# Optimization experiments

Measured on AMD Instinct MI355X. Metric: run time of the kernel, lower is better.

The kernel has to match this reference:

```python
import jax, jax.numpy as jnp
import numpy as np

N_TASK = 50000
N_PROC = 256
N_EDGES = 800000
EMB = 64
HEADS = 4
NLAYERS = 3
EDIM = 8
TDIM = 16
PDIM = 8
NGRAPHS = 8


def setup_inputs():
    key = jax.random.key(0)
    ks = jax.random.split(key, 30)

    def nrm(k, shape, fan_in):
        return jax.random.normal(k, shape, jnp.float32) / np.float32(np.sqrt(fan_in))

    inp = {}
    inp["x_task"] = jax.random.normal(ks[0], (N_TASK, TDIM), jnp.float32)
    inp["x_proc"] = jax.random.normal(ks[1], (N_PROC, PDIM), jnp.float32)
    inp["edge_index"] = jax.random.randint(ks[2], (2, N_EDGES), 0, N_TASK, dtype=jnp.int32)
    inp["edge_attr"] = jax.random.uniform(ks[3], (N_EDGES, EDIM), jnp.float32)
    inp["task_batch"] = jnp.sort(jax.random.randint(ks[4], (N_TASK,), 0, NGRAPHS, dtype=jnp.int32))
    inp["proc_batch"] = jnp.sort(jax.random.randint(ks[5], (N_PROC,), 0, NGRAPHS, dtype=jnp.int32))
    # input embeds
    inp["W_task"] = nrm(ks[6], (TDIM, EMB), TDIM)
    inp["b_task"] = jnp.zeros((EMB,), jnp.float32)
    inp["W_proc"] = nrm(ks[7], (PDIM, EMB), PDIM)
    inp["b_proc"] = jnp.zeros((EMB,), jnp.float32)
    # per-layer GAT params (stacked over layers)
    inp["gat_W"] = nrm(ks[8], (NLAYERS, EMB, HEADS * EMB), EMB)
    inp["gat_We"] = nrm(ks[9], (NLAYERS, EDIM, HEADS * EMB), EDIM)
    inp["att_src"] = nrm(ks[10], (NLAYERS, HEADS, EMB), EMB)
    inp["att_dst"] = nrm(ks[11], (NLAYERS, HEADS, EMB), EMB)
    inp["att_edge"] = nrm(ks[12], (NLAYERS, HEADS, EMB), EMB)
    inp["gat_b"] = jnp.zeros((NLAYERS, HEADS * EMB), jnp.float32)
    inp["proj_W"] = nrm(ks[13], (NLAYERS, HEADS * EMB, EMB), HEADS * EMB)
    inp["proj_b"] = jnp.zeros((NLAYERS, EMB), jnp.float32)
    inp["ln_g"] = jnp.ones((NLAYERS, EMB), jnp.float32)
    inp["ln_b"] = jnp.zeros((NLAYERS, EMB), jnp.float32)
    # heads
    inp["pt_W1"] = nrm(ks[14], (EMB, EMB // 2), EMB)
    inp["pt_b1"] = jnp.zeros((EMB // 2,), jnp.float32)
    inp["pt_W2"] = nrm(ks[15], (EMB // 2, 1), EMB // 2)
    inp["pt_b2"] = jnp.zeros((1,), jnp.float32)
    inp["v_W1"] = nrm(ks[16], (2 * EMB, EMB), 2 * EMB)
    inp["v_b1"] = jnp.zeros((EMB,), jnp.float32)
    inp["v_W2"] = nrm(ks[17], (EMB, 1), EMB)
    inp["v_b2"] = jnp.zeros((1,), jnp.float32)
    return inp


def _gat_layer(x, src, dst, eattr, W, We, a_s, a_d, a_e, bias):
    # PyG GATConv(in=-1 shared lin, heads=H, concat=True, edge_dim) with self loops already appended
    n = x.shape[0]
    xl = (x @ W).reshape(n, HEADS, EMB)            # [N,H,D]
    el = (eattr @ We).reshape(-1, HEADS, EMB)      # [E,H,D]
    a_src = jnp.einsum("nhd,hd->nh", xl, a_s)
    a_dst = jnp.einsum("nhd,hd->nh", xl, a_d)
    a_edg = jnp.einsum("ehd,hd->eh", el, a_e)
    alpha = jax.nn.leaky_relu(a_src[src] + a_dst[dst] + a_edg, 0.2)  # [E,H]
    m = jax.ops.segment_max(alpha, dst, num_segments=n)
    ex = jnp.exp(alpha - m[dst])
    denom = jax.ops.segment_sum(ex, dst, num_segments=n)
    coeff = ex / (denom[dst] + 1e-16)
    out = jax.ops.segment_sum(coeff[:, :, None] * xl[src], dst, num_segments=n)
    return out.reshape(n, HEADS * EMB) + bias


def _mean_pool(x, batch, g):
    s = jax.ops.segment_sum(x, batch, num_segments=g)
    cnt = jax.ops.segment_sum(jnp.ones((x.shape[0], 1), x.dtype), batch, num_segments=g)
    return s / jnp.maximum(cnt, 1.0)


def reference(x_task, x_proc, edge_attr, W_task, b_task, W_proc, b_proc, gat_W, gat_We,
              att_src, att_dst, att_edge, gat_b, proj_W, proj_b, ln_g, ln_b,
              pt_W1, pt_b1, pt_W2, pt_b2, v_W1, v_b1, v_W2, v_b2,
              edge_index, task_batch, proc_batch):
    h_t = x_task @ W_task + b_task
    h_p = x_proc @ W_proc + b_proc
    # add self loops; self-loop edge_attr = mean of edge_attr (PyG fill_value='mean')
    loop = jnp.arange(N_TASK, dtype=edge_index.dtype)
    src = jnp.concatenate([edge_index[0], loop])
    dst = jnp.concatenate([edge_index[1], loop])
    ea = jnp.concatenate([edge_attr, jnp.broadcast_to(edge_attr.mean(0), (N_TASK, EDIM))], axis=0)
    for l in range(NLAYERS):
        upd = _gat_layer(h_t, src, dst, ea, gat_W[l], gat_We[l], att_src[l], att_dst[l], att_edge[l], gat_b[l])
        upd = jax.nn.elu(upd @ proj_W[l] + proj_b[l])
        h = h_t + upd
        mu = h.mean(-1, keepdims=True)
        var = ((h - mu) ** 2).mean(-1, keepdims=True)
        h_t = (h - mu) / jnp.sqrt(var + 1e-5) * ln_g[l] + ln_b[l]
    task_logits = (jax.nn.relu(h_t @ pt_W1 + pt_b1) @ pt_W2 + pt_b2)[:, 0]
    tp = _mean_pool(h_t, task_batch, NGRAPHS)
    pp = _mean_pool(h_p, proc_batch, NGRAPHS)
    ge = jnp.concatenate([tp, pp], axis=1)
    value = jax.nn.relu(ge @ v_W1 + v_b1) @ v_W2 + v_b2
    return task_logits, value, h_t, h_p
```

## Files before the change

kernel.cpp:

```cpp
#include <hip/hip_runtime.h>
#include <hip/hip_bf16.h>
#include <math.h>

#define NT 50000
#define NP 256
#define NE 800000
#define ET 850000
#define EMBD 64
#define NHEADS 4
#define HE 256
#define NG 8
#define NBLK 49

typedef __attribute__((ext_vector_type(8))) short bf16x8;
typedef __attribute__((ext_vector_type(4))) float f32x4;

#define OFF_DEG    0u
#define OFF_INDPTR 200192u
#define OFF_CURSOR 400384u
#define OFF_BLKSUM 600576u
#define OFF_MG     600832u
#define OFF_MH     601216u
#define OFF_MEAN   601280u
#define OFF_TPSUM  601344u
#define OFF_TPCNT  603392u
#define OFF_SRCS   603648u
#define OFF_AE0    4003648u
#define OFF_AE1    17603648u
#define OFF_AE2    31203648u
#define OFF_ASRC   44803648u
#define OFF_ADST   45604416u
#define OFF_HT     46405184u
#define OFF_HTB    59217472u
#define OFF_XL     65623616u
#define OFF_AGG    91223616u
#define OFF_WXF    116848192u
#define OFF_WPF    116946496u

__device__ __forceinline__ float bf_lo(unsigned int u) {
  union { unsigned int i; float f; } v; v.i = u << 16; return v.f;
}
__device__ __forceinline__ float bf_hi(unsigned int u) {
  union { unsigned int i; float f; } v; v.i = u & 0xffff0000u; return v.f;
}

__global__ __launch_bounds__(256) void k_embed_task(const float* __restrict__ x,
    const float* __restrict__ W, const float* __restrict__ b,
    float* __restrict__ ht, __hip_bfloat16* __restrict__ htb) {
  int lane = threadIdx.x & 63, wid = threadIdx.x >> 6;
  float breg[16];
  #pragma unroll
  for (int k = 0; k < 16; k++) breg[k] = W[k * 64 + lane];
  float bias = b[lane];
  int row0 = blockIdx.x * 64 + wid * 16;
  #pragma unroll 1
  for (int r = 0; r < 16; r++) {
    int row = row0 + r;
    if (row >= NT) return;
    const float4* xr = (const float4*)(x + (size_t)row * 16);
    float acc = bias;
    #pragma unroll
    for (int q = 0; q < 4; q++) {
      float4 v = xr[q];
      acc += v.x * breg[q*4+0] + v.y * breg[q*4+1] + v.z * breg[q*4+2] + v.w * breg[q*4+3];
    }
    ht[(size_t)row * 64 + lane] = acc;
    htb[(size_t)row * 64 + lane] = __float2bfloat16(acc);
  }
}

__global__ __launch_bounds__(256) void k_degree_mean(const int* __restrict__ ei1,
    const float* __restrict__ ea, int* __restrict__ deg, float* __restrict__ sums) {
  __shared__ float lds[256];
  int tid = threadIdx.x;
  int e = blockIdx.x * 256 + tid;
  if (e < ET) {
    int d = (e < NE) ? ei1[e] : (e - NE);
    atomicAdd(&deg[d], 1);
  }
  int k = tid & 7, rl = tid >> 3;
  float s = 0.f;
  for (int row = blockIdx.x * 32 + rl; row < NE; row += gridDim.x * 32)
    s += ea[(size_t)row * 8 + k];
  lds[tid] = s;
  __syncthreads();
  for (int off = 128; off >= 8; off >>= 1) {
    if (tid < off) lds[tid] += lds[tid + off];
    __syncthreads();
  }
  if (tid < 8) atomicAdd(&sums[tid], lds[tid]);
}

__global__ __launch_bounds__(1024) void k_scanA(const int* __restrict__ deg,
    int* __restrict__ indptr, int* __restrict__ blksum) {
  __shared__ int wsum[16];
  int tid = threadIdx.x, lane = tid & 63, wid = tid >> 6;
  int i = blockIdx.x * 1024 + tid;
  int v = (i < NT) ? deg[i] : 0;
  int x = v;
  #pragma unroll
  for (int off = 1; off < 64; off <<= 1) {
    int t = __shfl_up(x, off, 64);
    if (lane >= off) x += t;
  }
  if (lane == 63) wsum[wid] = x;
  __syncthreads();
  if (wid == 0 && lane < 16) {
    int w = wsum[lane];
    #pragma unroll
    for (int off = 1; off < 16; off <<= 1) {
      int t = __shfl_up(w, off, 64);
      if (lane >= off) w += t;
    }
    wsum[lane] = w;
  }
  __syncthreads();
  int woff = (wid == 0) ? 0 : wsum[wid - 1];
  if (i < NT) indptr[i] = x + woff - v;
  if (tid == 1023) blksum[blockIdx.x] = wsum[15];
}

__global__ __launch_bounds__(1024) void k_scanB(const int* __restrict__ blksum,
    int* __restrict__ indptr, int* __restrict__ cursor) {
  __shared__ int bs[NBLK];
  int tid = threadIdx.x;
  if (tid < NBLK) bs[tid] = blksum[tid];
  __syncthreads();
  int off = 0;
  for (int j = 0; j < (int)blockIdx.x; j++) off += bs[j];
  int i = blockIdx.x * 1024 + tid;
  if (i < NT) {
    int e = indptr[i] + off;
    indptr[i] = e;
    cursor[i] = e;
  }
  if (blockIdx.x == 0 && tid == 0) {
    int tot = 0;
    for (int j = 0; j < NBLK; j++) tot += bs[j];
    indptr[NT] = tot;
  }
}

__global__ __launch_bounds__(128) void k_mprep(const float* __restrict__ We,
    const float* __restrict__ ae, const float* __restrict__ msum,
    float* __restrict__ Mg, float* __restrict__ Mh) {
  int t = threadIdx.x;
  if (t < 96) {
    int l = t >> 5, idx = t & 31, k = idx >> 2, h = idx & 3;
    const float* Wl = We + (size_t)l * 8 * HE;
    const float* al = ae + (size_t)l * NHEADS * EMBD;
    float s = 0.f;
    #pragma unroll
    for (int d = 0; d < 64; d++) s += Wl[k * HE + h * 64 + d] * al[h * 64 + d];
    Mg[t] = s;
  }
  __syncthreads();
  if (t < 12) {
    int l = t >> 2, h = t & 3;
    float m = 0.f;
    #pragma unroll
    for (int k = 0; k < 8; k++) m += msum[k] * (1.f / NE) * Mg[l * 32 + k * 4 + h];
    Mh[t] = m;
  }
}

__global__ __launch_bounds__(256) void k_fill(const int* __restrict__ ei0,
    const int* __restrict__ ei1, const float* __restrict__ ea,
    const float* __restrict__ Mg, const float* __restrict__ Mh,
    int* __restrict__ cursor, int* __restrict__ srcs,
    float4* __restrict__ ae0, float4* __restrict__ ae1, float4* __restrict__ ae2) {
  __shared__ float MgS[96];
  __shared__ float MhS[12];
  int t = threadIdx.x;
  if (t < 96) MgS[t] = Mg[t];
  if (t < 12) MhS[t] = Mh[t];
  __syncthreads();
  int e = blockIdx.x * 256 + t;
  if (e >= ET) return;
  int d, s;
  float4 r[3];
  if (e < NE) {
    d = ei1[e]; s = ei0[e];
    const float4* pp = (const float4*)(ea + (size_t)e * 8);
    float4 v0 = pp[0], v1 = pp[1];
    float v[8] = {v0.x, v0.y, v0.z, v0.w, v1.x, v1.y, v1.z, v1.w};
    #pragma unroll
    for (int l = 0; l < 3; l++) {
      float rr[4];
      #pragma unroll
      for (int h = 0; h < 4; h++) {
        float acc = 0.f;
        #pragma unroll
        for (int k = 0; k < 8; k++) acc += v[k] * MgS[l * 32 + k * 4 + h];
        rr[h] = acc;
      }
      r[l].x = rr[0]; r[l].y = rr[1]; r[l].z = rr[2]; r[l].w = rr[3];
    }
  } else {
    d = e - NE; s = d;
    #pragma unroll
    for (int l = 0; l < 3; l++) {
      r[l].x = MhS[l * 4 + 0]; r[l].y = MhS[l * 4 + 1];
      r[l].z = MhS[l * 4 + 2]; r[l].w = MhS[l * 4 + 3];
    }
  }
  int p = atomicAdd(&cursor[d], 1);
  srcs[p] = s;
  ae0[p] = r[0];
  ae1[p] = r[1];
  ae2[p] = r[2];
}

__global__ void k_prep_w(const float* __restrict__ Wx, const float* __restrict__ Wp,
                         __hip_bfloat16* __restrict__ Wxf, __hip_bfloat16* __restrict__ Wpf) {
  int lane = threadIdx.x;
  int bid = blockIdx.x;
  int quad = lane >> 4, l15 = lane & 15;
  if (bid < 96) {
    int l = bid >> 5, rem = bid & 31, t = rem >> 1, kb = rem & 1;
    const float* Wl = Wx + (size_t)l * 64 * 256;
    __hip_bfloat16* out = Wxf + (size_t)l * 16384 + (size_t)((t * 2 + kb) * 64 + lane) * 8;
    #pragma unroll
    for (int j = 0; j < 8; j++)
      out[j] = __float2bfloat16(Wl[(kb * 32 + quad * 8 + j) * 256 + t * 16 + l15]);
  } else {
    bid -= 96;
    int l = bid >> 5, rem = bid & 31, t = rem >> 3, kb = rem & 7;
    const float* Wl = Wp + (size_t)l * 256 * 64;
    __hip_bfloat16* out = Wpf + (size_t)l * 16384 + (size_t)((t * 8 + kb) * 64 + lane) * 8;
    #pragma unroll
    for (int j = 0; j < 8; j++)
      out[j] = __float2bfloat16(Wl[(kb * 32 + quad * 8 + j) * 64 + t * 16 + l15]);
  }
}

__global__ __launch_bounds__(256) void k_xl_mfma(
    const __hip_bfloat16* __restrict__ htb, const __hip_bfloat16* __restrict__ Wf,
    const float* __restrict__ as, const float* __restrict__ ad,
    __hip_bfloat16* __restrict__ xl, float* __restrict__ a_src, float* __restrict__ a_dst) {
  int lane = threadIdx.x & 63, wave = threadIdx.x >> 6;
  int quad = lane >> 4, l15 = lane & 15;
  int r0 = blockIdx.x * 64 + wave * 16;
  f32x4 acc[16];
  #pragma unroll
  for (int t = 0; t < 16; t++) acc[t] = (f32x4){0.f, 0.f, 0.f, 0.f};
  #pragma unroll
  for (int kb = 0; kb < 2; kb++) {
    bf16x8 a = *(const bf16x8*)(htb + (size_t)(r0 + l15) * 64 + kb * 32 + quad * 8);
    #pragma unroll
    for (int t = 0; t < 16; t++) {
      bf16x8 bfr = *(const bf16x8*)(Wf + (size_t)((t * 2 + kb) * 64 + lane) * 8);
      acc[t] = __builtin_amdgcn_mfma_f32_16x16x32_bf16(a, bfr, acc[t], 0, 0, 0);
    }
  }
  float asv[16], adv[16];
  #pragma unroll
  for (int t = 0; t < 16; t++) { asv[t] = as[t * 16 + l15]; adv[t] = ad[t * 16 + l15]; }
  #pragma unroll
  for (int reg = 0; reg < 4; reg++) {
    int row = r0 + quad * 4 + reg;
    bool ok = row < NT;
    float vs[4] = {0.f, 0.f, 0.f, 0.f}, vd[4] = {0.f, 0.f, 0.f, 0.f};
    #pragma unroll
    for (int t = 0; t < 16; t++) {
      float v = acc[t][reg];
      if (ok) xl[(size_t)row * HE + t * 16 + l15] = __float2bfloat16(v);
      vs[t >> 2] += v * asv[t];
      vd[t >> 2] += v * adv[t];
    }
    #pragma unroll
    for (int off = 8; off; off >>= 1) {
      #pragma unroll
      for (int h = 0; h < 4; h++) {
        vs[h] += __shfl_xor(vs[h], off, 64);
        vd[h] += __shfl_xor(vd[h], off, 64);
      }
    }
    if (ok && l15 == 0) {
      float4 s4; s4.x = vs[0]; s4.y = vs[1]; s4.z = vs[2]; s4.w = vs[3];
      float4 d4; d4.x = vd[0]; d4.y = vd[1]; d4.z = vd[2]; d4.w = vd[3];
      *(float4*)(a_src + (size_t)row * 4) = s4;
      *(float4*)(a_dst + (size_t)row * 4) = d4;
    }
  }
}

__global__ __launch_bounds__(256) void k_attn(
    const __hip_bfloat16* __restrict__ xl, const float* __restrict__ a_src,
    const float* __restrict__ a_dst, const float* __restrict__ aedg,
    const int* __restrict__ indptr, const int* __restrict__ srcs,
    const float* __restrict__ gb, __hip_bfloat16* __restrict__ agg) {
  int node = blockIdx.x * 4 + (threadIdx.x >> 6);
  int lane = threadIdx.x & 63;
  int h = lane >> 4;
  int hbase = lane & 48;
  int e15 = lane & 15;
  int beg = indptr[node], end = indptr[node + 1];
  float adh = a_dst[node * 4 + h];
  float M = -1e30f, S = 0.f;
  float acc0 = 0.f, acc1 = 0.f, acc2 = 0.f, acc3 = 0.f;
  for (int base = beg; base < end; base += 16) {
    int cnt = min(16, end - base);
    int el = base + e15;
    bool ok = e15 < cnt;
    int my_src = ok ? srcs[el] : 0;
    float aeh = ok ? aedg[(size_t)el * 4 + h] : 0.f;
    float asr = ok ? a_src[(size_t)my_src * 4 + h] : 0.f;
    float al = asr + adh + aeh;
    al = (al > 0.f) ? al : 0.2f * al;
    if (!ok) al = -1e30f;
    float cm = al;
    #pragma unroll
    for (int off = 1; off < 16; off <<= 1) cm = fmaxf(cm, __shfl_xor(cm, off, 64));
    float newM = fmaxf(M, cm);
    float corr = __expf(M - newM);
    float ex = __expf(al - newM);
    float cs = ex;
    #pragma unroll
    for (int off = 1; off < 16; off <<= 1) cs += __shfl_xor(cs, off, 64);
    S = S * corr + cs;
    M = newM;
    acc0 *= corr; acc1 *= corr; acc2 *= corr; acc3 *= corr;
    if (cnt == 16) {
      #pragma unroll 4
      for (int j = 0; j < 16; j++) {
        int src = __shfl(my_src, j, 64);
        float cf = __shfl(ex, hbase | j, 64);
        uint2 u = *(const uint2*)(xl + (size_t)src * HE + lane * 4);
        acc0 += cf * bf_lo(u.x);
        acc1 += cf * bf_hi(u.x);
        acc2 += cf * bf_lo(u.y);
        acc3 += cf * bf_hi(u.y);
      }
    } else {
      for (int j = 0; j < cnt; j++) {
        int src = __shfl(my_src, j, 64);
        float cf = __shfl(ex, hbase | j, 64);
        uint2 u = *(const uint2*)(xl + (size_t)src * HE + lane * 4);
        acc0 += cf * bf_lo(u.x);
        acc1 += cf * bf_hi(u.x);
        acc2 += cf * bf_lo(u.y);
        acc3 += cf * bf_hi(u.y);
      }
    }
  }
  float inv = 1.f / (S + 1e-16f);
  float4 g4 = *(const float4*)(gb + lane * 4);
  unsigned int o0 = __bfloat16_as_ushort(__float2bfloat16(acc0 * inv + g4.x));
  unsigned int o1 = __bfloat16_as_ushort(__float2bfloat16(acc1 * inv + g4.y));
  unsigned int o2 = __bfloat16_as_ushort(__float2bfloat16(acc2 * inv + g4.z));
  unsigned int o3 = __bfloat16_as_ushort(__float2bfloat16(acc3 * inv + g4.w));
  uint2 out; out.x = o0 | (o1 << 16); out.y = o2 | (o3 << 16);
  *(uint2*)(agg + (size_t)node * HE + lane * 4) = out;
}

__global__ __launch_bounds__(256) void k_proj_mfma(
    const __hip_bfloat16* __restrict__ agg, const __hip_bfloat16* __restrict__ Wf,
    const float* __restrict__ pb, const float* __restrict__ g, const float* __restrict__ b,
    const float* __restrict__ ht_in, float* __restrict__ ht_out,
    __hip_bfloat16* __restrict__ htb_out, int writebf) {
  int lane = threadIdx.x & 63, wave = threadIdx.x >> 6;
  int quad = lane >> 4, l15 = lane & 15;
  int r0 = blockIdx.x * 64 + wave * 16;
  f32x4 acc[4];
  #pragma unroll
  for (int t = 0; t < 4; t++) acc[t] = (f32x4){0.f, 0.f, 0.f, 0.f};
  #pragma unroll
  for (int kb = 0; kb < 8; kb++) {
    bf16x8 a = *(const bf16x8*)(agg + (size_t)(r0 + l15) * HE + kb * 32 + quad * 8);
    #pragma unroll
    for (int t = 0; t < 4; t++) {
      bf16x8 bfr = *(const bf16x8*)(Wf + (size_t)((t * 8 + kb) * 64 + lane) * 8);
      acc[t] = __builtin_amdgcn_mfma_f32_16x16x32_bf16(a, bfr, acc[t], 0, 0, 0);
    }
  }
  float pbv[4], gv[4], bv[4];
  #pragma unroll
  for (int t = 0; t < 4; t++) {
    pbv[t] = pb[t * 16 + l15];
    gv[t] = g[t * 16 + l15];
    bv[t] = b[t * 16 + l15];
  }
  #pragma unroll
  for (int reg = 0; reg < 4; reg++) {
    int row = r0 + quad * 4 + reg;
    bool ok = row < NT;
    float h[4], rs = 0.f;
    #pragma unroll
    for (int t = 0; t < 4; t++) {
      float u = acc[t][reg] + pbv[t];
      u = (u > 0.f) ? u : (__expf(u) - 1.f);
      h[t] = ht_in[(size_t)row * 64 + t * 16 + l15] + u;
      rs += h[t];
    }
    #pragma unroll
    for (int off = 8; off; off >>= 1) rs += __shfl_xor(rs, off, 64);
    float mu = rs * 0.015625f;
    float vv = 0.f;
    #pragma unroll
    for (int t = 0; t < 4; t++) { float d = h[t] - mu; vv += d * d; }
    #pragma unroll
    for (int off = 8; off; off >>= 1) vv += __shfl_xor(vv, off, 64);
    float rstd = rsqrtf(vv * 0.015625f + 1e-5f);
    #pragma unroll
    for (int t = 0; t < 4; t++) {
      float o = (h[t] - mu) * rstd * gv[t] + bv[t];
      if (ok) {
        ht_out[(size_t)row * 64 + t * 16 + l15] = o;
        if (writebf) htb_out[(size_t)row * 64 + t * 16 + l15] = __float2bfloat16(o);
      }
    }
  }
}

__global__ __launch_bounds__(256) void k_task_head(const float* __restrict__ ht,
    const float* __restrict__ W1, const float* __restrict__ b1,
    const float* __restrict__ W2, const float* __restrict__ b2, float* __restrict__ logits) {
  __shared__ float lh[8 * 64];
  int t = threadIdx.x;
  size_t base = (size_t)blockIdx.x * 8 * 64;
  lh[t] = ht[base + t];
  lh[t + 256] = ht[base + t + 256];
  __syncthreads();
  int i = t >> 5, j = t & 31;
  float s = b1[j];
  #pragma unroll 8
  for (int d = 0; d < 64; d++) s += lh[i * 64 + d] * W1[d * 32 + j];
  s = fmaxf(s, 0.f);
  float p = s * W2[j];
  #pragma unroll
  for (int off = 16; off; off >>= 1) p += __shfl_xor(p, off, 64);
  if (j == 0) logits[blockIdx.x * 8 + i] = p + b2[0];
}

__global__ __launch_bounds__(256) void k_pool_task(const float* __restrict__ ht,
    const int* __restrict__ tb, float* __restrict__ sums, float* __restrict__ cnt) {
  int lane = threadIdx.x & 63, sub = threadIdx.x >> 6;
  float acc[8], c[8];
  #pragma unroll
  for (int g = 0; g < 8; g++) { acc[g] = 0.f; c[g] = 0.f; }
  int lim = min(NT, (int)((blockIdx.x + 1) * 512));
  for (int n = blockIdx.x * 512 + sub; n < lim; n += 4) {
    int g = tb[n];
    float v = ht[(size_t)n * 64 + lane];
    #pragma unroll
    for (int gg = 0; gg < 8; gg++) {
      if (g == gg) { acc[gg] += v; c[gg] += 1.f; }
    }
  }
  #pragma unroll
  for (int g = 0; g < 8; g++) {
    if (__any(acc[g] != 0.f || c[g] != 0.f)) {
      atomicAdd(&sums[g * 64 + lane], acc[g]);
      if (lane == 0) atomicAdd(&cnt[g], c[g]);
    }
  }
}

__global__ __launch_bounds__(512) void k_value(const float* __restrict__ tpsum,
    const float* __restrict__ tpcnt, const float* __restrict__ x_proc,
    const float* __restrict__ W_proc, const float* __restrict__ b_proc,
    float* __restrict__ hp_out, const int* __restrict__ pbatch,
    const float* __restrict__ vW1, const float* __restrict__ vb1,
    const float* __restrict__ vW2, const float* __restrict__ vb2,
    float* __restrict__ val_out) {
  __shared__ float ge[8 * 128];
  int t = threadIdx.x;
  int g = t >> 6, d = t & 63;
  float wreg[8];
  #pragma unroll
  for (int k = 0; k < 8; k++) wreg[k] = W_proc[k * 64 + d];
  float bd = b_proc[d];
  for (int p = g; p < 256; p += 8) {
    const float* xr = x_proc + (size_t)p * 8;
    float a = bd;
    #pragma unroll
    for (int k = 0; k < 8; k++) a += xr[k] * wreg[k];
    hp_out[(size_t)p * 64 + d] = a;
  }
  __syncthreads();
  float c = fmaxf(tpcnt[g], 1.f);
  ge[g * 128 + d] = tpsum[g * 64 + d] / c;
  float s = 0.f, cc = 0.f;
  for (int p = 0; p < 256; p++) {
    int bg = pbatch[p];
    if (bg == g) { s += hp_out[(size_t)p * 64 + d]; cc += 1.f; }
  }
  ge[g * 128 + 64 + d] = s / fmaxf(cc, 1.f);
  __syncthreads();
  float acc = vb1[d];
  #pragma unroll 8
  for (int k = 0; k < 128; k++) acc += ge[g * 128 + k] * vW1[k * 64 + d];
  acc = fmaxf(acc, 0.f);
  float p = acc * vW2[d];
  #pragma unroll
  for (int off = 32; off; off >>= 1) p += __shfl_xor(p, off, 64);
  if (d == 0) val_out[g] = p + vb2[0];
}

extern "C" void kernel_launch(void* const* d_in, const int* in_sizes, int n_in,
                              void* d_out, int out_size, void* d_ws, size_t ws_size,
                              hipStream_t stream) {
  (void)in_sizes; (void)n_in; (void)out_size; (void)ws_size;
  const float* x_task  = (const float*)d_in[0];
  const float* x_proc  = (const float*)d_in[1];
  const int*   eidx    = (const int*)d_in[2];
  const float* eattr   = (const float*)d_in[3];
  const int*   tbatch  = (const int*)d_in[4];
  const int*   pbatch  = (const int*)d_in[5];
  const float* W_task  = (const float*)d_in[6];
  const float* b_task  = (const float*)d_in[7];
  const float* W_proc  = (const float*)d_in[8];
  const float* b_proc  = (const float*)d_in[9];
  const float* gat_W   = (const float*)d_in[10];
  const float* gat_We  = (const float*)d_in[11];
  const float* att_src = (const float*)d_in[12];
  const float* att_dst = (const float*)d_in[13];
  const float* att_edge= (const float*)d_in[14];
  const float* gat_b   = (const float*)d_in[15];
  const float* proj_W  = (const float*)d_in[16];
  const float* proj_b  = (const float*)d_in[17];
  const float* ln_g    = (const float*)d_in[18];
  const float* ln_b    = (const float*)d_in[19];
  const float* pt_W1   = (const float*)d_in[20];
  const float* pt_b1   = (const float*)d_in[21];
  const float* pt_W2   = (const float*)d_in[22];
  const float* pt_b2   = (const float*)d_in[23];
  const float* v_W1    = (const float*)d_in[24];
  const float* v_b1    = (const float*)d_in[25];
  const float* v_W2    = (const float*)d_in[26];
  const float* v_b2    = (const float*)d_in[27];

  char* ws = (char*)d_ws;
  int*   deg    = (int*)(ws + OFF_DEG);
  int*   indptr = (int*)(ws + OFF_INDPTR);
  int*   cursor = (int*)(ws + OFF_CURSOR);
  int*   blksum = (int*)(ws + OFF_BLKSUM);
  float* Mg     = (float*)(ws + OFF_MG);
  float* Mh     = (float*)(ws + OFF_MH);
  float* msum   = (float*)(ws + OFF_MEAN);
  float* tpsum  = (float*)(ws + OFF_TPSUM);
  float* tpcnt  = (float*)(ws + OFF_TPCNT);
  int*   srcs   = (int*)(ws + OFF_SRCS);
  float4* ae0   = (float4*)(ws + OFF_AE0);
  float4* ae1   = (float4*)(ws + OFF_AE1);
  float4* ae2   = (float4*)(ws + OFF_AE2);
  float* a_src  = (float*)(ws + OFF_ASRC);
  float* a_dst  = (float*)(ws + OFF_ADST);
  float* ht     = (float*)(ws + OFF_HT);
  __hip_bfloat16* htb = (__hip_bfloat16*)(ws + OFF_HTB);
  __hip_bfloat16* xl  = (__hip_bfloat16*)(ws + OFF_XL);
  __hip_bfloat16* agg = (__hip_bfloat16*)(ws + OFF_AGG);
  __hip_bfloat16* wxf = (__hip_bfloat16*)(ws + OFF_WXF);
  __hip_bfloat16* wpf = (__hip_bfloat16*)(ws + OFF_WPF);
  float* aedg[3] = {(float*)ae0, (float*)ae1, (float*)ae2};

  float* out_logits = (float*)d_out;
  float* out_value  = (float*)d_out + NT;
  float* out_ht     = (float*)d_out + NT + NG;
  float* out_hp     = (float*)d_out + NT + NG + (size_t)NT * EMBD;

  hipMemsetAsync(ws + OFF_DEG, 0, NT * 4, stream);
  hipMemsetAsync(ws + OFF_MEAN, 0, 2144, stream);

  k_embed_task<<<782, 256, 0, stream>>>(x_task, W_task, b_task, ht, htb);
  k_degree_mean<<<(ET + 255) / 256, 256, 0, stream>>>(eidx + NE, eattr, deg, msum);
  k_scanA<<<NBLK, 1024, 0, stream>>>(deg, indptr, blksum);
  k_scanB<<<NBLK, 1024, 0, stream>>>(blksum, indptr, cursor);
  k_mprep<<<1, 128, 0, stream>>>(gat_We, att_edge, msum, Mg, Mh);
  k_fill<<<(ET + 255) / 256, 256, 0, stream>>>(eidx, eidx + NE, eattr, Mg, Mh,
                                               cursor, srcs, ae0, ae1, ae2);
  k_prep_w<<<192, 64, 0, stream>>>(gat_W, proj_W, wxf, wpf);

  for (int l = 0; l < 3; l++) {
    k_xl_mfma<<<782, 256, 0, stream>>>(htb, wxf + (size_t)l * 16384,
                                       att_src + l * NHEADS * EMBD,
                                       att_dst + l * NHEADS * EMBD,
                                       xl, a_src, a_dst);
    k_attn<<<NT / 4, 256, 0, stream>>>(xl, a_src, a_dst, aedg[l], indptr, srcs,
                                       gat_b + l * HE, agg);
    float* htout = (l == 2) ? out_ht : ht;
    k_proj_mfma<<<782, 256, 0, stream>>>(agg, wpf + (size_t)l * 16384,
                                         proj_b + l * EMBD, ln_g + l * EMBD,
                                         ln_b + l * EMBD, ht, htout, htb,
                                         (l == 2) ? 0 : 1);
  }

  k_task_head<<<NT / 8, 256, 0, stream>>>(out_ht, pt_W1, pt_b1, pt_W2, pt_b2, out_logits);
  k_pool_task<<<(NT + 511) / 512, 256, 0, stream>>>(out_ht, tbatch, tpsum, tpcnt);
  k_value<<<1, 512, 0, stream>>>(tpsum, tpcnt, x_proc, W_proc, b_proc, out_hp,
                                 pbatch, v_W1, v_b1, v_W2, v_b2, out_value);
}
```

Baseline: 719.8 us.

## Pack edge src and bf16 logits into one record; stage MFMA outputs through LDS

```diff
diff --git a/kernel.cpp b/kernel.cpp
--- a/kernel.cpp
+++ b/kernel.cpp
@@ -24,24 +24,28 @@
 #define OFF_MEAN   601280u
 #define OFF_TPSUM  601344u
 #define OFF_TPCNT  603392u
-#define OFF_SRCS   603648u
-#define OFF_AE0    4003648u
-#define OFF_AE1    17603648u
-#define OFF_AE2    31203648u
-#define OFF_ASRC   44803648u
-#define OFF_ADST   45604416u
-#define OFF_HT     46405184u
-#define OFF_HTB    59217472u
-#define OFF_XL     65623616u
-#define OFF_AGG    91223616u
-#define OFF_WXF    116848192u
-#define OFF_WPF    116946496u
+#define OFF_ER0    603648u
+#define OFF_ER1    14203648u
+#define OFF_ER2    27803648u
+#define OFF_ASRC   41403648u
+#define OFF_ADST   42204416u
+#define OFF_HT     43005184u
+#define OFF_HTB    55817472u
+#define OFF_XL     62223616u
+#define OFF_AGG    87823616u
+#define OFF_WXF    113448192u
+#define OFF_WPF    113546496u
 
 __device__ __forceinline__ float bf_lo(unsigned int u) {
   union { unsigned int i; float f; } v; v.i = u << 16; return v.f;
 }
 __device__ __forceinline__ float bf_hi(unsigned int u) {
   union { unsigned int i; float f; } v; v.i = u & 0xffff0000u; return v.f;
+}
+__device__ __forceinline__ unsigned pk2(float a, float b) {
+  unsigned ua = __bfloat16_as_ushort(__float2bfloat16(a));
+  unsigned ub = __bfloat16_as_ushort(__float2bfloat16(b));
+  return ua | (ub << 16);
 }
 
 __global__ __launch_bounds__(256) void k_embed_task(const float* __restrict__ x,
@@ -167,8 +171,8 @@
 __global__ __launch_bounds__(256) void k_fill(const int* __restrict__ ei0,
     const int* __restrict__ ei1, const float* __restrict__ ea,
     const float* __restrict__ Mg, const float* __restrict__ Mh,
-    int* __restrict__ cursor, int* __restrict__ srcs,
-    float4* __restrict__ ae0, float4* __restrict__ ae1, float4* __restrict__ ae2) {
+    int* __restrict__ cursor,
+    uint4* __restrict__ er0, uint4* __restrict__ er1, uint4* __restrict__ er2) {
   __shared__ float MgS[96];
   __shared__ float MhS[12];
   int t = threadIdx.x;
@@ -178,7 +182,7 @@
   int e = blockIdx.x * 256 + t;
   if (e >= ET) return;
   int d, s;
-  float4 r[3];
+  float r[3][4];
   if (e < NE) {
     d = ei1[e]; s = ei0[e];
     const float4* pp = (const float4*)(ea + (size_t)e * 8);
@@ -186,29 +190,27 @@
     float v[8] = {v0.x, v0.y, v0.z, v0.w, v1.x, v1.y, v1.z, v1.w};
     #pragma unroll
     for (int l = 0; l < 3; l++) {
-      float rr[4];
       #pragma unroll
       for (int h = 0; h < 4; h++) {
         float acc = 0.f;
         #pragma unroll
         for (int k = 0; k < 8; k++) acc += v[k] * MgS[l * 32 + k * 4 + h];
-        rr[h] = acc;
+        r[l][h] = acc;
       }
-      r[l].x = rr[0]; r[l].y = rr[1]; r[l].z = rr[2]; r[l].w = rr[3];
     }
   } else {
     d = e - NE; s = d;
     #pragma unroll
-    for (int l = 0; l < 3; l++) {
-      r[l].x = MhS[l * 4 + 0]; r[l].y = MhS[l * 4 + 1];
-      r[l].z = MhS[l * 4 + 2]; r[l].w = MhS[l * 4 + 3];
-    }
+    for (int l = 0; l < 3; l++)
+      #pragma unroll
+      for (int h = 0; h < 4; h++) r[l][h] = MhS[l * 4 + h];
   }
   int p = atomicAdd(&cursor[d], 1);
-  srcs[p] = s;
-  ae0[p] = r[0];
-  ae1[p] = r[1];
-  ae2[p] = r[2];
+  uint4 rc;
+  rc.x = (unsigned)s; rc.w = 0u;
+  rc.y = pk2(r[0][0], r[0][1]); rc.z = pk2(r[0][2], r[0][3]); er0[p] = rc;
+  rc.y = pk2(r[1][0], r[1][1]); rc.z = pk2(r[1][2], r[1][3]); er1[p] = rc;
+  rc.y = pk2(r[2][0], r[2][1]); rc.z = pk2(r[2][2], r[2][3]); er2[p] = rc;
 }
 
 __global__ void k_prep_w(const float* __restrict__ Wx, const float* __restrict__ Wp,
@@ -238,58 +240,71 @@
     const __hip_bfloat16* __restrict__ htb, const __hip_bfloat16* __restrict__ Wf,
     const float* __restrict__ as, const float* __restrict__ ad,
     __hip_bfloat16* __restrict__ xl, float* __restrict__ a_src, float* __restrict__ a_dst) {
-  int lane = threadIdx.x & 63, wave = threadIdx.x >> 6;
+  __shared__ __hip_bfloat16 cbuf[64 * 264];
+  __shared__ float asL[256], adL[256];
+  int tid = threadIdx.x;
+  int lane = tid & 63, wave = tid >> 6;
   int quad = lane >> 4, l15 = lane & 15;
-  int r0 = blockIdx.x * 64 + wave * 16;
+  asL[tid] = as[tid];
+  adL[tid] = ad[tid];
+  int r0 = blockIdx.x * 64;
+  int arow = r0 + wave * 16 + l15;
   f32x4 acc[16];
   #pragma unroll
   for (int t = 0; t < 16; t++) acc[t] = (f32x4){0.f, 0.f, 0.f, 0.f};
   #pragma unroll
   for (int kb = 0; kb < 2; kb++) {
-    bf16x8 a = *(const bf16x8*)(htb + (size_t)(r0 + l15) * 64 + kb * 32 + quad * 8);
+    bf16x8 a = *(const bf16x8*)(htb + (size_t)arow * 64 + kb * 32 + quad * 8);
     #pragma unroll
     for (int t = 0; t < 16; t++) {
       bf16x8 bfr = *(const bf16x8*)(Wf + (size_t)((t * 2 + kb) * 64 + lane) * 8);
       acc[t] = __builtin_amdgcn_mfma_f32_16x16x32_bf16(a, bfr, acc[t], 0, 0, 0);
     }
   }
-  float asv[16], adv[16];
-  #pragma unroll
-  for (int t = 0; t < 16; t++) { asv[t] = as[t * 16 + l15]; adv[t] = ad[t * 16 + l15]; }
-  #pragma unroll
-  for (int reg = 0; reg < 4; reg++) {
-    int row = r0 + quad * 4 + reg;
-    bool ok = row < NT;
-    float vs[4] = {0.f, 0.f, 0.f, 0.f}, vd[4] = {0.f, 0.f, 0.f, 0.f};
-    #pragma unroll
-    for (int t = 0; t < 16; t++) {
-      float v = acc[t][reg];
-      if (ok) xl[(size_t)row * HE + t * 16 + l15] = __float2bfloat16(v);
-      vs[t >> 2] += v * asv[t];
-      vd[t >> 2] += v * adv[t];
-    }
-    #pragma unroll
-    for (int off = 8; off; off >>= 1) {
-      #pragma unroll
-      for (int h = 0; h < 4; h++) {
-        vs[h] += __shfl_xor(vs[h], off, 64);
-        vd[h] += __shfl_xor(vd[h], off, 64);
-      }
-    }
-    if (ok && l15 == 0) {
-      float4 s4; s4.x = vs[0]; s4.y = vs[1]; s4.z = vs[2]; s4.w = vs[3];
-      float4 d4; d4.x = vd[0]; d4.y = vd[1]; d4.z = vd[2]; d4.w = vd[3];
-      *(float4*)(a_src + (size_t)row * 4) = s4;
-      *(float4*)(a_dst + (size_t)row * 4) = d4;
+  int rloc = wave * 16 + quad * 4;
+  #pragma unroll
+  for (int t = 0; t < 16; t++) {
+    #pragma unroll
+    for (int reg = 0; reg < 4; reg++)
+      cbuf[(rloc + reg) * 264 + t * 16 + l15] = __float2bfloat16(acc[t][reg]);
+  }
+  __syncthreads();
+  {
+    int r = tid & 63, q = tid >> 6;
+    const __hip_bfloat16* rowp = &cbuf[r * 264 + q * 64];
+    float vs = 0.f, vd = 0.f;
+    #pragma unroll
+    for (int d8 = 0; d8 < 8; d8++) {
+      uint4 u = *(const uint4*)(rowp + d8 * 8);
+      float x0 = bf_lo(u.x), x1 = bf_hi(u.x), x2 = bf_lo(u.y), x3 = bf_hi(u.y);
+      float x4 = bf_lo(u.z), x5 = bf_hi(u.z), x6 = bf_lo(u.w), x7 = bf_hi(u.w);
+      const float* ap = &asL[q * 64 + d8 * 8];
+      const float* dp = &adL[q * 64 + d8 * 8];
+      vs += x0*ap[0]+x1*ap[1]+x2*ap[2]+x3*ap[3]+x4*ap[4]+x5*ap[5]+x6*ap[6]+x7*ap[7];
+      vd += x0*dp[0]+x1*dp[1]+x2*dp[2]+x3*dp[3]+x4*dp[4]+x5*dp[5]+x6*dp[6]+x7*dp[7];
+    }
+    int row = r0 + r;
+    if (row < NT) {
+      a_src[row * 4 + q] = vs;
+      a_dst[row * 4 + q] = vd;
+    }
+  }
+  #pragma unroll
+  for (int k = 0; k < 8; k++) {
+    int c = k * 256 + tid;
+    int row = c >> 5, off = c & 31;
+    if (r0 + row < NT) {
+      uint4 v = *(const uint4*)(&cbuf[row * 264 + off * 8]);
+      *(uint4*)(xl + (size_t)(r0 + row) * HE + off * 8) = v;
     }
   }
 }
 
 __global__ __launch_bounds__(256) void k_attn(
     const __hip_bfloat16* __restrict__ xl, const float* __restrict__ a_src,
-    const float* __restrict__ a_dst, const float* __restrict__ aedg,
-    const int* __restrict__ indptr, const int* __restrict__ srcs,
-    const float* __restrict__ gb, __hip_bfloat16* __restrict__ agg) {
+    const float* __restrict__ a_dst, const uint4* __restrict__ er,
+    const int* __restrict__ indptr, const float* __restrict__ gb,
+    __hip_bfloat16* __restrict__ agg) {
   int node = blockIdx.x * 4 + (threadIdx.x >> 6);
   int lane = threadIdx.x & 63;
   int h = lane >> 4;
@@ -301,10 +316,12 @@
   float acc0 = 0.f, acc1 = 0.f, acc2 = 0.f, acc3 = 0.f;
   for (int base = beg; base < end; base += 16) {
     int cnt = min(16, end - base);
-    int el = base + e15;
     bool ok = e15 < cnt;
-    int my_src = ok ? srcs[el] : 0;
-    float aeh = ok ? aedg[(size_t)el * 4 + h] : 0.f;
+    uint4 rec; rec.x = 0u; rec.y = 0u; rec.z = 0u; rec.w = 0u;
+    if (ok) rec = er[base + e15];
+    int my_src = (int)rec.x;
+    unsigned wsel = (h < 2) ? rec.y : rec.z;
+    float aeh = (h & 1) ? bf_hi(wsel) : bf_lo(wsel);
     float asr = ok ? a_src[(size_t)my_src * 4 + h] : 0.f;
     float al = asr + adh + aeh;
     al = (al > 0.f) ? al : 0.2f * al;
@@ -359,56 +376,81 @@
     const float* __restrict__ pb, const float* __restrict__ g, const float* __restrict__ b,
     const float* __restrict__ ht_in, float* __restrict__ ht_out,
     __hip_bfloat16* __restrict__ htb_out, int writebf) {
-  int lane = threadIdx.x & 63, wave = threadIdx.x >> 6;
+  __shared__ float cbuf[64 * 68];
+  __shared__ float red[8 * 64];
+  __shared__ float stats[2 * 64];
+  __shared__ float pbL[64], gL[64], bL[64];
+  int tid = threadIdx.x;
+  int lane = tid & 63, wave = tid >> 6;
   int quad = lane >> 4, l15 = lane & 15;
-  int r0 = blockIdx.x * 64 + wave * 16;
+  if (tid < 64) { pbL[tid] = pb[tid]; gL[tid] = g[tid]; bL[tid] = b[tid]; }
+  int r0 = blockIdx.x * 64;
+  int arow = r0 + wave * 16 + l15;
   f32x4 acc[4];
   #pragma unroll
   for (int t = 0; t < 4; t++) acc[t] = (f32x4){0.f, 0.f, 0.f, 0.f};
   #pragma unroll
   for (int kb = 0; kb < 8; kb++) {
-    bf16x8 a = *(const bf16x8*)(agg + (size_t)(r0 + l15) * HE + kb * 32 + quad * 8);
+    bf16x8 a = *(const bf16x8*)(agg + (size_t)arow * HE + kb * 32 + quad * 8);
     #pragma unroll
     for (int t = 0; t < 4; t++) {
       bf16x8 bfr = *(const bf16x8*)(Wf + (size_t)((t * 8 + kb) * 64 + lane) * 8);
       acc[t] = __builtin_amdgcn_mfma_f32_16x16x32_bf16(a, bfr, acc[t], 0, 0, 0);
     }
   }
-  float pbv[4], gv[4], bv[4];
+  int rloc = wave * 16 + quad * 4;
   #pragma unroll
   for (int t = 0; t < 4; t++) {
-    pbv[t] = pb[t * 16 + l15];
-    gv[t] = g[t * 16 + l15];
-    bv[t] = b[t * 16 + l15];
-  }
-  #pragma unroll
-  for (int reg = 0; reg < 4; reg++) {
-    int row = r0 + quad * 4 + reg;
-    bool ok = row < NT;
-    float h[4], rs = 0.f;
-    #pragma unroll
-    for (int t = 0; t < 4; t++) {
-      float u = acc[t][reg] + pbv[t];
-      u = (u > 0.f) ? u : (__expf(u) - 1.f);
-      h[t] = ht_in[(size_t)row * 64 + t * 16 + l15] + u;
-      rs += h[t];
-    }
-    #pragma unroll
-    for (int off = 8; off; off >>= 1) rs += __shfl_xor(rs, off, 64);
-    float mu = rs * 0.015625f;
-    float vv = 0.f;
-    #pragma unroll
-    for (int t = 0; t < 4; t++) { float d = h[t] - mu; vv += d * d; }
-    #pragma unroll
-    for (int off = 8; off; off >>= 1) vv += __shfl_xor(vv, off, 64);
-    float rstd = rsqrtf(vv * 0.015625f + 1e-5f);
-    #pragma unroll
-    for (int t = 0; t < 4; t++) {
-      float o = (h[t] - mu) * rstd * gv[t] + bv[t];
-      if (ok) {
-        ht_out[(size_t)row * 64 + t * 16 + l15] = o;
-        if (writebf) htb_out[(size_t)row * 64 + t * 16 + l15] = __float2bfloat16(o);
-      }
+    #pragma unroll
+    for (int reg = 0; reg < 4; reg++)
+      cbuf[(rloc + reg) * 68 + t * 16 + l15] = acc[t][reg];
+  }
+  __syncthreads();
+  int r = tid >> 2, q = tid & 3;
+  int row = r0 + r;
+  float h[16];
+  float s1 = 0.f, s2 = 0.f;
+  const float* hin = ht_in + (size_t)row * 64 + q * 16;
+  #pragma unroll
+  for (int d = 0; d < 16; d++) {
+    float u = cbuf[r * 68 + q * 16 + d] + pbL[q * 16 + d];
+    u = (u > 0.f) ? u : (__expf(u) - 1.f);
+    float hv = hin[d] + u;
+    h[d] = hv;
+    s1 += hv; s2 += hv * hv;
+  }
+  red[q * 64 + r] = s1;
+  red[256 + q * 64 + r] = s2;
+  __syncthreads();
+  if (tid < 64) {
+    float sa = red[tid] + red[64 + tid] + red[128 + tid] + red[192 + tid];
+    float sb = red[256 + tid] + red[320 + tid] + red[384 + tid] + red[448 + tid];
+    float mu = sa * 0.015625f;
+    float var = sb * 0.015625f - mu * mu;
+    stats[tid] = mu;
+    stats[64 + tid] = rsqrtf(var + 1e-5f);
+  }
+  __syncthreads();
+  float mu = stats[r], rstd = stats[64 + r];
+  if (row < NT) {
+    float o[16];
+    #pragma unroll
+    for (int d = 0; d < 16; d++)
+      o[d] = (h[d] - mu) * rstd * gL[q * 16 + d] + bL[q * 16 + d];
+    float* outp = ht_out + (size_t)row * 64 + q * 16;
+    #pragma unroll
+    for (int d4 = 0; d4 < 4; d4++) {
+      float4 v; v.x = o[d4*4]; v.y = o[d4*4+1]; v.z = o[d4*4+2]; v.w = o[d4*4+3];
+      *(float4*)(outp + d4 * 4) = v;
+    }
+    if (writebf) {
+      uint4 u0, u1;
+      u0.x = pk2(o[0], o[1]);  u0.y = pk2(o[2], o[3]);
+      u0.z = pk2(o[4], o[5]);  u0.w = pk2(o[6], o[7]);
+      u1.x = pk2(o[8], o[9]);  u1.y = pk2(o[10], o[11]);
+      u1.z = pk2(o[12], o[13]); u1.w = pk2(o[14], o[15]);
+      uint4* hb = (uint4*)(htb_out + (size_t)row * 64 + q * 16);
+      hb[0] = u0; hb[1] = u1;
     }
   }
 }
@@ -541,10 +583,9 @@
   float* msum   = (float*)(ws + OFF_MEAN);
   float* tpsum  = (float*)(ws + OFF_TPSUM);
   float* tpcnt  = (float*)(ws + OFF_TPCNT);
-  int*   srcs   = (int*)(ws + OFF_SRCS);
-  float4* ae0   = (float4*)(ws + OFF_AE0);
-  float4* ae1   = (float4*)(ws + OFF_AE1);
-  float4* ae2   = (float4*)(ws + OFF_AE2);
+  uint4* er0    = (uint4*)(ws + OFF_ER0);
+  uint4* er1    = (uint4*)(ws + OFF_ER1);
+  uint4* er2    = (uint4*)(ws + OFF_ER2);
   float* a_src  = (float*)(ws + OFF_ASRC);
   float* a_dst  = (float*)(ws + OFF_ADST);
   float* ht     = (float*)(ws + OFF_HT);
@@ -553,7 +594,7 @@
   __hip_bfloat16* agg = (__hip_bfloat16*)(ws + OFF_AGG);
   __hip_bfloat16* wxf = (__hip_bfloat16*)(ws + OFF_WXF);
   __hip_bfloat16* wpf = (__hip_bfloat16*)(ws + OFF_WPF);
-  float* aedg[3] = {(float*)ae0, (float*)ae1, (float*)ae2};
+  uint4* ers[3] = {er0, er1, er2};
 
   float* out_logits = (float*)d_out;
   float* out_value  = (float*)d_out + NT;
@@ -569,7 +610,7 @@
   k_scanB<<<NBLK, 1024, 0, stream>>>(blksum, indptr, cursor);
   k_mprep<<<1, 128, 0, stream>>>(gat_We, att_edge, msum, Mg, Mh);
   k_fill<<<(ET + 255) / 256, 256, 0, stream>>>(eidx, eidx + NE, eattr, Mg, Mh,
-                                               cursor, srcs, ae0, ae1, ae2);
+                                               cursor, er0, er1, er2);
   k_prep_w<<<192, 64, 0, stream>>>(gat_W, proj_W, wxf, wpf);
 
   for (int l = 0; l < 3; l++) {
@@ -577,7 +618,7 @@
                                        att_src + l * NHEADS * EMBD,
                                        att_dst + l * NHEADS * EMBD,
                                        xl, a_src, a_dst);
-    k_attn<<<NT / 4, 256, 0, stream>>>(xl, a_src, a_dst, aedg[l], indptr, srcs,
+    k_attn<<<NT / 4, 256, 0, stream>>>(xl, a_src, a_dst, ers[l], indptr,
                                        gat_b + l * HE, agg);
     float* htout = (l == 2) ? out_ht : ht;
     k_proj_mfma<<<782, 256, 0, stream>>>(agg, wpf + (size_t)l * 16384,
```

After: 694.6 us. 1.04x faster.
